# Kernel tuning notes

Hardware: AMD Instinct MI355X
Metric: run time of the kernel (lower is better)

Reference implementation:

```python
import jax, jax.numpy as jnp
import numpy as np

B, NO, Q = 128, 36, 14          # batch, num object regions, question length
VD, QD, H = 2048, 1024, 2048    # v_dim, q_dim, FCNet hidden dim


def setup_inputs() -> dict:
    key = jax.random.key(0)
    ks = jax.random.split(key, 10)
    s = lambda fan_in: 1.0 / np.sqrt(fan_in)
    return {
        "v": jax.random.normal(ks[0], (B, NO, VD), dtype=jnp.float32),
        "q": jax.random.normal(ks[1], (B, Q, QD), dtype=jnp.float32),
        # v_net: weight_norm Linear(v_dim, 2048) + ReLU (effective weight)
        "Wv": jax.random.normal(ks[2], (H, VD), dtype=jnp.float32) * s(VD),
        "bv": jax.random.normal(ks[3], (H,), dtype=jnp.float32) * 0.01,
        # q_net: weight_norm Linear(q_dim, 2048) + ReLU
        "Wq": jax.random.normal(ks[4], (H, QD), dtype=jnp.float32) * s(QD),
        "bq": jax.random.normal(ks[5], (H,), dtype=jnp.float32) * 0.01,
        # h_net: Linear(14, 1) applied along the question axis of d_
        "wh": jax.random.normal(ks[6], (Q,), dtype=jnp.float32) * s(Q),
        "bh": jax.random.normal(ks[7], (), dtype=jnp.float32) * 0.01,
        # h_net2: Linear(v_dim, v_dim) == Linear(2048, 2048)
        "W2": jax.random.normal(ks[8], (VD, H), dtype=jnp.float32) * s(H),
        "b2": jax.random.normal(ks[9], (VD,), dtype=jnp.float32) * 0.01,
    }


def reference(v, q, Wv, bv, Wq, bq, wh, bh, W2, b2):
    # FCNet (eval mode: dropout = identity): ReLU(weight-norm Linear)
    v_ = jax.nn.relu(jnp.einsum("bnd,hd->bnh", v, Wv) + bv)  # [B, NO, H]
    q_ = jax.nn.relu(jnp.einsum("bqd,hd->bqh", q, Wq) + bq)  # [B, Q,  H]
    # Original: d_[b,h,n,q] = v_[b,n,h] * q_[b,q,h]; logits = h_net(d_)
    # => logits[b,h,n] = sum_q v_[b,n,h] * q_[b,q,h] * wh[q] + bh
    # Fused: reduce q_ against wh first, avoiding the [B,H,NO,Q] intermediate.
    qw = jnp.einsum("bqh,q->bh", q_, wh)                     # [B, H]
    logits = v_ * qw[:, None, :] + bh                        # [B, NO, H]
    # h_net2 on last dim
    return jnp.einsum("bnh,vh->bnv", logits, W2) + b2        # [B, NO, VD]
```

## Files before the change

### kernel.cpp

```cpp
#include <hip/hip_runtime.h>
#include <hip/hip_bf16.h>


typedef __attribute__((ext_vector_type(4))) float f32x4;
typedef __attribute__((ext_vector_type(8))) short short8;

__device__ __forceinline__ short f2bf(float f) {
    union { float f; unsigned u; } x; x.f = f;
    unsigned u = x.u;
    unsigned r = (u + 0x7FFFu + ((u >> 16) & 1u)) >> 16;
    return (short)(r & 0xFFFFu);
}
__device__ __forceinline__ float bf2f(short s) {
    union { unsigned u; float f; } x; x.u = ((unsigned)(unsigned short)s) << 16;
    return x.f;
}

__device__ __forceinline__ void gload_lds16(const short* g, short* l) {
    __builtin_amdgcn_global_load_lds(
        (const __attribute__((address_space(1))) unsigned int*)g,
        (__attribute__((address_space(3))) unsigned int*)l,
        16, 0, 0);
}

__device__ __forceinline__ void cvt_chunk(const float* __restrict__ src,
                                          short* __restrict__ dst, int i)
{
    f32x4 a = *(const f32x4*)&src[i];
    f32x4 b = *(const f32x4*)&src[i + 4];
    short8 s;
    #pragma unroll
    for (int j = 0; j < 4; ++j) { s[j] = f2bf(a[j]); s[4 + j] = f2bf(b[j]); }
    *(short8*)&dst[i] = s;
}

#define Q_CH  229376
#define QW_CH 262144
__global__ __launch_bounds__(256)
void cvt_qw(const float* __restrict__ q,  short* __restrict__ qb,
            const float* __restrict__ Wq, short* __restrict__ Wqb)
{
    const int total = Q_CH + QW_CH;
    const int stride = gridDim.x * 256;
    for (int c = blockIdx.x * 256 + threadIdx.x; c < total; c += stride) {
        if (c < Q_CH) cvt_chunk(q, qb, c * 8);
        else          cvt_chunk(Wq, Wqb, (c - Q_CH) * 8);
    }
}

#define V_CH  1179648
#define WV_CH 524288
#define W2_CH 524288
__global__ __launch_bounds__(256)
void k1_fused(const short* __restrict__ Ab, const short* __restrict__ Bb,
              const float* __restrict__ bias, short* __restrict__ Cp,
              const float* __restrict__ v,  short* __restrict__ vb,
              const float* __restrict__ Wv, short* __restrict__ Wvb,
              const float* __restrict__ W2, short* __restrict__ W2b)
{
    __shared__ short ldsA[128 * 64];
    __shared__ short ldsB[128 * 64];

    if (blockIdx.x >= 224) {
        const int total = V_CH + WV_CH + W2_CH;
        const int stride = 288 * 256;
        for (int c = (blockIdx.x - 224) * 256 + threadIdx.x; c < total; c += stride) {
            if      (c < V_CH)         cvt_chunk(v,  vb,  c * 8);
            else if (c < V_CH + WV_CH) cvt_chunk(Wv, Wvb, (c - V_CH) * 8);
            else                       cvt_chunk(W2, W2b, (c - V_CH - WV_CH) * 8);
        }
        return;
    }

    const int K = 1024, N = 2048;
    const int tid    = threadIdx.x;
    const int lane   = tid & 63;
    const int wid    = tid >> 6;
    const int wr     = wid >> 1;
    const int wc     = wid & 1;
    const int lrow   = lane & 15;
    const int lchunk = lane >> 4;

    const int row0 = (blockIdx.x % 14) * 128;
    const int col0 = (blockIdx.x / 14) * 128;

    const int s_r = lane >> 3;
    const int s_c = ((lane & 7) ^ s_r) * 8;

    f32x4 acc[4][4];
    #pragma unroll
    for (int i = 0; i < 4; ++i)
        #pragma unroll
        for (int j = 0; j < 4; ++j)
            acc[i][j] = (f32x4)0.0f;

    const int nk = K >> 6;

    for (int kt = 0; kt < nk; ++kt) {
        const int kc = kt * 64;
        if (kt) __syncthreads();
        #pragma unroll
        for (int i = 0; i < 4; ++i) {
            const int r = wid * 32 + i * 8 + s_r;
            gload_lds16(&Ab[(size_t)(row0 + r) * K + kc + s_c],
                        &ldsA[(wid * 32 + i * 8) * 64]);
            gload_lds16(&Bb[(size_t)(col0 + r) * K + kc + s_c],
                        &ldsB[(wid * 32 + i * 8) * 64]);
        }
        __syncthreads();

        short8 af[4][2], bfv[4][2];
        #pragma unroll
        for (int mi = 0; mi < 4; ++mi) {
            const int row = wr * 64 + mi * 16 + lrow;
            #pragma unroll
            for (int ks = 0; ks < 2; ++ks)
                af[mi][ks] = *(const short8*)((const char*)ldsA +
                    row * 128 + (((ks * 4 + lchunk) * 16) ^ ((row & 7) << 4)));
        }
        #pragma unroll
        for (int ni = 0; ni < 4; ++ni) {
            const int row = wc * 64 + ni * 16 + lrow;
            #pragma unroll
            for (int ks = 0; ks < 2; ++ks)
                bfv[ni][ks] = *(const short8*)((const char*)ldsB +
                    row * 128 + (((ks * 4 + lchunk) * 16) ^ ((row & 7) << 4)));
        }
        #pragma unroll
        for (int ks = 0; ks < 2; ++ks)
            #pragma unroll
            for (int mi = 0; mi < 4; ++mi)
                #pragma unroll
                for (int ni = 0; ni < 4; ++ni)
                    acc[mi][ni] = __builtin_amdgcn_mfma_f32_16x16x32_bf16(
                        af[mi][ks], bfv[ni][ks], acc[mi][ni], 0, 0, 0);
    }

    #pragma unroll
    for (int mi = 0; mi < 4; ++mi)
        #pragma unroll
        for (int ni = 0; ni < 4; ++ni)
            #pragma unroll
            for (int r = 0; r < 4; ++r) {
                const int row = row0 + wr * 64 + mi * 16 + lchunk * 4 + r;
                const int col = col0 + wc * 64 + ni * 16 + lrow;
                float val = fmaxf(acc[mi][ni][r] + bias[col], 0.0f);
                Cp[(size_t)row * N + col] = f2bf(val);
            }
}

template<int EPI>
__global__ __launch_bounds__(512, 2)
void gemm256(const short* __restrict__ Ab, const short* __restrict__ Bb,
             const float* __restrict__ bias, const float* __restrict__ qw,
             const float* __restrict__ bh_p, void* __restrict__ Cp,
             int M, int N, int K)
{
    __shared__ short lds[2][4][128 * 64];

    const int tid  = threadIdx.x;
    const int lane = tid & 63;
    const int w    = tid >> 6;
    const int wr   = w >> 2;
    const int wc   = w & 3;
    const int fr   = lane & 15;
    const int fc   = lane >> 4;

    const int row0 = blockIdx.x * 256;
    const int col0 = blockIdx.y * 256;

    const int sl_s = lane >> 3;
    const int sl_c = ((lane & 7) ^ sl_s) * 8;

    const int nt = K >> 6;

    f32x4 acc[8][4];
    #pragma unroll
    for (int i = 0; i < 8; ++i)
        #pragma unroll
        for (int j = 0; j < 4; ++j)
            acc[i][j] = (f32x4)0.0f;

    auto stageA = [&](int t, int q) {
        #pragma unroll
        for (int i = 0; i < 2; ++i) {
            const int g  = w * 2 + i;
            const int rl = g * 8 + sl_s;
            const int srow = row0 + (g >> 3) * 128 + q * 64 + (rl & 63);
            gload_lds16(&Ab[(size_t)srow * K + t * 64 + sl_c],
                        &lds[t & 1][q][g * 512]);
        }
    };
    auto stageB = [&](int t, int q) {
        #pragma unroll
        for (int i = 0; i < 2; ++i) {
            const int g  = w * 2 + i;
            const int rl = g * 8 + sl_s;
            const int srow = col0 + (rl >> 5) * 64 + q * 32 + (rl & 31);
            gload_lds16(&Bb[(size_t)srow * K + t * 64 + sl_c],
                        &lds[t & 1][2 + q][g * 512]);
        }
    };

    short8 A0[4][2], A1[4][2], B0[2][2], B1[2][2];

#define READA(T, MQ, DST)                                                       \
    _Pragma("unroll") for (int m_ = 0; m_ < 4; ++m_) {                          \
        const int rl_ = wr * 64 + m_ * 16 + fr;                                 \
        _Pragma("unroll") for (int k_ = 0; k_ < 2; ++k_)                        \
            DST[m_][k_] = *(const short8*)((const char*)&lds[(T) & 1][MQ][0]    \
                + rl_ * 128 + ((k_ * 64 + fc * 16) ^ ((rl_ & 7) << 4)));        \
    }
#define READB(T, NQ, DST)                                                       \
    _Pragma("unroll") for (int n_ = 0; n_ < 2; ++n_) {                          \
        const int rl_ = wc * 32 + n_ * 16 + fr;                                 \
        _Pragma("unroll") for (int k_ = 0; k_ < 2; ++k_)                        \
            DST[n_][k_] = *(const short8*)((const char*)&lds[(T) & 1][2 + (NQ)][0] \
                + rl_ * 128 + ((k_ * 64 + fc * 16) ^ ((rl_ & 7) << 4)));        \
    }
#define MFMAQ(MQ, NQ, ASET, BSET)                                               \
    _Pragma("unroll") for (int m_ = 0; m_ < 4; ++m_)                            \
      _Pragma("unroll") for (int n_ = 0; n_ < 2; ++n_)                          \
        _Pragma("unroll") for (int k_ = 0; k_ < 2; ++k_)                        \
          acc[(MQ) * 4 + m_][(NQ) * 2 + n_] =                                   \
              __builtin_amdgcn_mfma_f32_16x16x32_bf16(                          \
                  ASET[m_][k_], BSET[n_][k_], acc[(MQ) * 4 + m_][(NQ) * 2 + n_], 0, 0, 0);

#define BAR()   asm volatile("s_barrier" ::: "memory")
#define PRIO1() __builtin_amdgcn_s_setprio(1)
#define PRIO0() __builtin_amdgcn_s_setprio(0)
#define VM4()   asm volatile("s_waitcnt vmcnt(4)" ::: "memory")
#define VM0()   asm volatile("s_waitcnt vmcnt(0)" ::: "memory")

#define KITER(T0, T1, ST1, ST2, ST3, ST4, ST5, ST6, ST7, ST8, D4, D8)           \
  {                                                                             \
    READA(T0, 0, A0); READB(T0, 0, B0);                                         \
    PRIO1(); MFMAQ(0, 0, A0, B0); PRIO0();                                      \
    READB(T0, 1, B1); ST1; BAR();                                               \
    PRIO1(); MFMAQ(0, 1, A0, B1); PRIO0();                                      \
    READA(T0, 1, A1); ST2; BAR();                                               \
    PRIO1(); MFMAQ(1, 1, A1, B1); PRIO0();                                      \
    ST3; BAR();                                                                 \
    PRIO1(); MFMAQ(1, 0, A1, B0); PRIO0();                                      \
    ST4; D4; BAR();                                                             \
    READA(T1, 0, A0); READB(T1, 0, B0);                                         \
    PRIO1(); MFMAQ(0, 0, A0, B0); PRIO0();                                      \
    READB(T1, 1, B1); ST5; BAR();                                               \
    PRIO1(); MFMAQ(0, 1, A0, B1); PRIO0();                                      \
    READA(T1, 1, A1); ST6; BAR();                                               \
    PRIO1(); MFMAQ(1, 1, A1, B1); PRIO0();                                      \
    ST7; BAR();                                                                 \
    PRIO1(); MFMAQ(1, 0, A1, B0); PRIO0();                                      \
    ST8; D8; BAR();                                                             \
  }

    stageA(0, 0); stageB(0, 0); stageB(0, 1); stageA(0, 1);
    stageA(1, 0); stageB(1, 1);
    VM4();
    BAR();

    const int niter = (nt >> 1) - 1;
    for (int j = 0; j < niter; ++j) {
        const int t0 = 2 * j, t1 = 2 * j + 1;
        KITER(t0, t1,
              stageA(t1, 1),     stageB(t1, 0),
              stageA(t0 + 2, 0), stageB(t0 + 2, 1),
              stageA(t0 + 2, 1), stageB(t0 + 2, 0),
              stageA(t1 + 2, 0), stageB(t1 + 2, 1),
              VM4(), VM4());
    }
    {
        const int t0 = nt - 2, t1 = nt - 1;
        KITER(t0, t1,
              stageA(t1, 1), stageB(t1, 0),
              (void)0, (void)0, (void)0, (void)0, (void)0, (void)0,
              VM0(), (void)0);
    }

#undef KITER
#undef READA
#undef READB
#undef MFMAQ
#undef BAR
#undef PRIO1
#undef PRIO0
#undef VM4
#undef VM0

    const float bhv = (EPI == 1) ? bh_p[0] : 0.0f;
    #pragma unroll
    for (int m = 0; m < 8; ++m) {
        #pragma unroll
        for (int n = 0; n < 4; ++n) {
            #pragma unroll
            for (int r = 0; r < 4; ++r) {
                const int row = row0 + wr * 128 + m * 16 + fc * 4 + r;
                const int col = col0 + wc * 64 + n * 16 + fr;
                float val = acc[m][n][r];
                if (EPI == 1) {
                    val = fmaxf(val + bias[col], 0.0f);
                    const int b = row / 36;
                    val = val * qw[b * 2048 + col] + bhv;
                    ((short*)Cp)[(size_t)row * N + col] = f2bf(val);
                } else {
                    ((float*)Cp)[(size_t)row * N + col] = val + bias[col];
                }
            }
        }
    }
}

__global__ __launch_bounds__(256)
void qw_reduce(const short* __restrict__ q_, const float* __restrict__ wh,
               float* __restrict__ qw)
{
    const int idx = blockIdx.x * 256 + threadIdx.x;
    const int b = idx >> 11;
    const int h = idx & 2047;
    float s = 0.0f;
    #pragma unroll
    for (int qq = 0; qq < 14; ++qq)
        s += bf2f(q_[(size_t)(b * 14 + qq) * 2048 + h]) * wh[qq];
    qw[idx] = s;
}

extern "C" void kernel_launch(void* const* d_in, const int* in_sizes, int n_in,
                              void* d_out, int out_size, void* d_ws, size_t ws_size,
                              hipStream_t stream)
{
    const float* v  = (const float*)d_in[0];
    const float* q  = (const float*)d_in[1];
    const float* Wv = (const float*)d_in[2];
    const float* bv = (const float*)d_in[3];
    const float* Wq = (const float*)d_in[4];
    const float* bq = (const float*)d_in[5];
    const float* wh = (const float*)d_in[6];
    const float* bh = (const float*)d_in[7];
    const float* W2 = (const float*)d_in[8];
    const float* b2 = (const float*)d_in[9];
    float* out = (float*)d_out;

    char* ws = (char*)d_ws;
    short* vb     = (short*)(ws);
    short* Wvb    = (short*)(ws + 18874368);
    short* W2b    = (short*)(ws + 27262976);
    short* qb     = (short*)(ws + 35651584);
    short* Wqb    = (short*)(ws + 39321600);
    short* q_ws   = (short*)(ws + 43515904);
    float* qw     = (float*)(ws + 50855936);
    short* logits = (short*)(ws + 51904512);

    cvt_qw<<<1024, 256, 0, stream>>>(q, qb, Wq, Wqb);

    k1_fused<<<512, 256, 0, stream>>>(qb, Wqb, bq, q_ws,
                                      v, vb, Wv, Wvb, W2, W2b);

    qw_reduce<<<(128 * 2048) / 256, 256, 0, stream>>>(q_ws, wh, qw);

    gemm256<1><<<dim3(4608 / 256, 2048 / 256), 512, 0, stream>>>(
        vb, Wvb, bv, qw, bh, logits, 4608, 2048, 2048);

    gemm256<2><<<dim3(4608 / 256, 2048 / 256), 512, 0, stream>>>(
        logits, W2b, b2, nullptr, nullptr, out, 4608, 2048, 2048);
}
```

Measured before the change: 140.7 us.

## Fuse qw reduction into GEMM prologue and restructure K-loop staging

Removes the separate qw_reduce kernel: each EPI==1 GEMM block now computes the q-weighted sums for its up to 8 batches and 256 columns into LDS before the main loop, and reads qw from LDS in the epilogue. The K-loop is also restructured from eight interleaved load/barrier phases per iteration to two half-phases per tile, issuing a full tile's stage loads at once with a deeper vmcnt(8) wait. This saves one launch and a global round-trip for qw, in exchange for redundant qw computation across column-blocks and a prologue delay before the GEMM starts. It also uses fewer barriers but gives coarser interleaving of loads with MFMAs.

```diff
diff --git a/kernel.cpp b/kernel.cpp
--- a/kernel.cpp
+++ b/kernel.cpp
@@ -152,11 +152,13 @@
 template<int EPI>
 __global__ __launch_bounds__(512, 2)
 void gemm256(const short* __restrict__ Ab, const short* __restrict__ Bb,
-             const float* __restrict__ bias, const float* __restrict__ qw,
+             const float* __restrict__ bias,
+             const short* __restrict__ q_, const float* __restrict__ whp,
              const float* __restrict__ bh_p, void* __restrict__ Cp,
              int M, int N, int K)
 {
     __shared__ short lds[2][4][128 * 64];
+    __shared__ float qw_lds[8][256];
 
     const int tid  = threadIdx.x;
     const int lane = tid & 63;
@@ -168,11 +170,29 @@
 
     const int row0 = blockIdx.x * 256;
     const int col0 = blockIdx.y * 256;
+    const int b_lo = row0 / 36;
 
     const int sl_s = lane >> 3;
     const int sl_c = ((lane & 7) ^ sl_s) * 8;
 
     const int nt = K >> 6;
+
+    if (EPI == 1) {
+        #pragma unroll
+        for (int i = 0; i < 4; ++i) {
+            const int idx = tid * 4 + i;
+            const int bb = idx >> 8, cc = idx & 255;
+            const int b = b_lo + bb;
+            float s = 0.0f;
+            if (b < 128) {
+                #pragma unroll
+                for (int qq = 0; qq < 14; ++qq)
+                    s += bf2f(q_[(size_t)(b * 14 + qq) * 2048 + col0 + cc]) * whp[qq];
+            }
+            qw_lds[bb][cc] = s;
+        }
+        __syncthreads();
+    }
 
     f32x4 acc[8][4];
     #pragma unroll
@@ -229,62 +249,50 @@
 #define BAR()   asm volatile("s_barrier" ::: "memory")
 #define PRIO1() __builtin_amdgcn_s_setprio(1)
 #define PRIO0() __builtin_amdgcn_s_setprio(0)
-#define VM4()   asm volatile("s_waitcnt vmcnt(4)" ::: "memory")
+#define VM8()   asm volatile("s_waitcnt vmcnt(8)" ::: "memory")
 #define VM0()   asm volatile("s_waitcnt vmcnt(0)" ::: "memory")
 
-#define KITER(T0, T1, ST1, ST2, ST3, ST4, ST5, ST6, ST7, ST8, D4, D8)           \
-  {                                                                             \
-    READA(T0, 0, A0); READB(T0, 0, B0);                                         \
+#define SPA(T)                                                                  \
+    READA(T, 0, A0); READB(T, 0, B0);                                           \
     PRIO1(); MFMAQ(0, 0, A0, B0); PRIO0();                                      \
-    READB(T0, 1, B1); ST1; BAR();                                               \
+    READB(T, 1, B1);                                                            \
     PRIO1(); MFMAQ(0, 1, A0, B1); PRIO0();                                      \
-    READA(T0, 1, A1); ST2; BAR();                                               \
-    PRIO1(); MFMAQ(1, 1, A1, B1); PRIO0();                                      \
-    ST3; BAR();                                                                 \
-    PRIO1(); MFMAQ(1, 0, A1, B0); PRIO0();                                      \
-    ST4; D4; BAR();                                                             \
-    READA(T1, 0, A0); READB(T1, 0, B0);                                         \
-    PRIO1(); MFMAQ(0, 0, A0, B0); PRIO0();                                      \
-    READB(T1, 1, B1); ST5; BAR();                                               \
-    PRIO1(); MFMAQ(0, 1, A0, B1); PRIO0();                                      \
-    READA(T1, 1, A1); ST6; BAR();                                               \
-    PRIO1(); MFMAQ(1, 1, A1, B1); PRIO0();                                      \
-    ST7; BAR();                                                                 \
-    PRIO1(); MFMAQ(1, 0, A1, B0); PRIO0();                                      \
-    ST8; D8; BAR();                                                             \
-  }
-
-    stageA(0, 0); stageB(0, 0); stageB(0, 1); stageA(0, 1);
-    stageA(1, 0); stageB(1, 1);
-    VM4();
+    READA(T, 1, A1);                                                            \
     BAR();
-
-    const int niter = (nt >> 1) - 1;
-    for (int j = 0; j < niter; ++j) {
+#define SPB(ST, D)                                                              \
+    ST;                                                                         \
+    PRIO1(); MFMAQ(1, 1, A1, B1); MFMAQ(1, 0, A1, B0); PRIO0();                 \
+    D; BAR();
+#define STAGE4(T) { stageA(T, 0); stageB(T, 0); stageB(T, 1); stageA(T, 1); }
+
+    STAGE4(0);
+    STAGE4(1);
+    VM8();
+    BAR();
+
+    const int niter = nt >> 1;
+    for (int j = 0; j < niter - 1; ++j) {
         const int t0 = 2 * j, t1 = 2 * j + 1;
-        KITER(t0, t1,
-              stageA(t1, 1),     stageB(t1, 0),
-              stageA(t0 + 2, 0), stageB(t0 + 2, 1),
-              stageA(t0 + 2, 1), stageB(t0 + 2, 0),
-              stageA(t1 + 2, 0), stageB(t1 + 2, 1),
-              VM4(), VM4());
-    }
-    {
-        const int t0 = nt - 2, t1 = nt - 1;
-        KITER(t0, t1,
-              stageA(t1, 1), stageB(t1, 0),
-              (void)0, (void)0, (void)0, (void)0, (void)0, (void)0,
-              VM0(), (void)0);
-    }
-
-#undef KITER
+        SPA(t0);
+        SPB(STAGE4(t0 + 2), VM8());
+        SPA(t1);
+        SPB(STAGE4(t1 + 2), VM8());
+    }
+    SPA(nt - 2);
+    SPB((void)0, VM0());
+    SPA(nt - 1);
+    PRIO1(); MFMAQ(1, 1, A1, B1); MFMAQ(1, 0, A1, B0); PRIO0();
+
+#undef SPA
+#undef SPB
+#undef STAGE4
 #undef READA
 #undef READB
 #undef MFMAQ
 #undef BAR
 #undef PRIO1
 #undef PRIO0
-#undef VM4
+#undef VM8
 #undef VM0
 
     const float bhv = (EPI == 1) ? bh_p[0] : 0.0f;
@@ -299,8 +307,7 @@
                 float val = acc[m][n][r];
                 if (EPI == 1) {
                     val = fmaxf(val + bias[col], 0.0f);
-                    const int b = row / 36;
-                    val = val * qw[b * 2048 + col] + bhv;
+                    val = val * qw_lds[row / 36 - b_lo][col - col0] + bhv;
                     ((short*)Cp)[(size_t)row * N + col] = f2bf(val);
                 } else {
                     ((float*)Cp)[(size_t)row * N + col] = val + bias[col];
@@ -308,20 +315,6 @@
             }
         }
     }
-}
-
-__global__ __launch_bounds__(256)
-void qw_reduce(const short* __restrict__ q_, const float* __restrict__ wh,
-               float* __restrict__ qw)
-{
-    const int idx = blockIdx.x * 256 + threadIdx.x;
-    const int b = idx >> 11;
-    const int h = idx & 2047;
-    float s = 0.0f;
-    #pragma unroll
-    for (int qq = 0; qq < 14; ++qq)
-        s += bf2f(q_[(size_t)(b * 14 + qq) * 2048 + h]) * wh[qq];
-    qw[idx] = s;
 }
 
 extern "C" void kernel_launch(void* const* d_in, const int* in_sizes, int n_in,
@@ -347,19 +340,16 @@
     short* qb     = (short*)(ws + 35651584);
     short* Wqb    = (short*)(ws + 39321600);
     short* q_ws   = (short*)(ws + 43515904);
-    float* qw     = (float*)(ws + 50855936);
-    short* logits = (short*)(ws + 51904512);
+    short* logits = (short*)(ws + 50855936);
 
     cvt_qw<<<1024, 256, 0, stream>>>(q, qb, Wq, Wqb);
 
     k1_fused<<<512, 256, 0, stream>>>(qb, Wqb, bq, q_ws,
                                       v, vb, Wv, Wvb, W2, W2b);
 
-    qw_reduce<<<(128 * 2048) / 256, 256, 0, stream>>>(q_ws, wh, qw);
-
     gemm256<1><<<dim3(4608 / 256, 2048 / 256), 512, 0, stream>>>(
-        vb, Wvb, bv, qw, bh, logits, 4608, 2048, 2048);
+        vb, Wvb, bv, q_ws, wh, bh, logits, 4608, 2048, 2048);
 
     gemm256<2><<<dim3(4608 / 256, 2048 / 256), 512, 0, stream>>>(
-        logits, W2b, b2, nullptr, nullptr, out, 4608, 2048, 2048);
-}
+        logits, W2b, b2, nullptr, nullptr, nullptr, out, 4608, 2048, 2048);
+}
```

After: 154.1 us. +9.6%, slower.
